# Kernel tuning notes

Measured on AMD Instinct MI355X. Metric: run time of the kernel, lower is better.

Reference implementation:

```python
import jax, jax.numpy as jnp
import numpy as np

N_NODES = 50000
N_EDGES = 600000
D = 128
H = 128


def setup_inputs() -> dict:
    key = jax.random.key(0)
    k1, k2, k3, k4 = jax.random.split(key, 4)
    x = jax.random.normal(k1, (N_NODES, D), dtype=jnp.float32)
    edge_index = jax.random.randint(k2, (2, N_EDGES), 0, N_NODES, dtype=jnp.int64)
    # Glorot-ish init for the two linear layers of SAGEConv
    scale = 1.0 / np.sqrt(D)
    W_l = jax.random.normal(k3, (H, D), dtype=jnp.float32) * scale
    b_l = jnp.zeros((H,), dtype=jnp.float32)
    W_r = jax.random.normal(k4, (H, D), dtype=jnp.float32) * scale
    return {"x": x, "edge_index": edge_index, "W_l": W_l, "b_l": b_l, "W_r": W_r}


def reference(x, edge_index, W_l, b_l, W_r):
    # PyG SAGEConv (aggr='mean', root_weight=True):
    #   out[i] = lin_l( mean_{j->i} x[j] ) + lin_r( x[i] )
    # edge_index[0] = source nodes (j), edge_index[1] = destination nodes (i)
    src = edge_index[0]
    dst = edge_index[1]
    n = x.shape[0]
    msgs = x[src]  # [E, D] gather
    agg_sum = jax.ops.segment_sum(msgs, dst, num_segments=n)  # [N, D]
    deg = jax.ops.segment_sum(jnp.ones((src.shape[0],), dtype=x.dtype), dst, num_segments=n)
    agg = agg_sum / jnp.maximum(deg, 1.0)[:, None]  # mean aggregation; 0 for isolated nodes
    out = agg @ W_l.T + b_l + x @ W_r.T  # [N, H]
    return out
```

## Files before the change

### kernel.cpp

```cpp
#include <hip/hip_runtime.h>
#include <hip/hip_bf16.h>

using f32x4 = __attribute__((ext_vector_type(4))) float;
using s16x8 = __attribute__((ext_vector_type(8))) short;

static __device__ __forceinline__ float bflo2f(unsigned int w) {
    union { unsigned int u; float f; } c; c.u = w << 16; return c.f;
}
static __device__ __forceinline__ float bfhi2f(unsigned int w) {
    union { unsigned int u; float f; } c; c.u = w & 0xffff0000u; return c.f;
}
static __device__ __forceinline__ unsigned int f2bf(float f) {
    union { float f; unsigned int u; } c; c.f = f;
    unsigned int u = c.u;
    u = u + 0x7fffu + ((u >> 16) & 1u);
    return u >> 16;
}

#define CAP 64

__global__ __launch_bounds__(256) void k_convert(
        const float* __restrict__ x, unsigned short* __restrict__ xb,
        const float* __restrict__ Wr, const float* __restrict__ Wl,
        s16x8* __restrict__ wprep, int* __restrict__ cnt, int* __restrict__ ovfn,
        int n4, int nxb, int N)
{
    int b = blockIdx.x;
    if (b < nxb) {
        int t = b * 256 + threadIdx.x;
        if (t >= n4) return;
        float4 v = ((const float4*)x)[t];
        ushort4 o;
        o.x = (unsigned short)f2bf(v.x);
        o.y = (unsigned short)f2bf(v.y);
        o.z = (unsigned short)f2bf(v.z);
        o.w = (unsigned short)f2bf(v.w);
        ((ushort4*)xb)[t] = o;
    } else if (b < nxb + 16) {
        int s = (b - nxb) * 256 + threadIdx.x;
        if (s >= 4096) return;
        int f = s >> 6, il = s & 63;
        int nt = f >> 3, ks = f & 7;
        int col = nt * 16 + (il & 15);
        int k   = ks * 32 + (il >> 4) * 8;
        const float* Wsrc = (k < 128) ? Wr : Wl;
        int k0 = k & 127;
        const float4* wp = (const float4*)(Wsrc + (size_t)col * 128 + k0);
        float4 w0 = wp[0], w1 = wp[1];
        s16x8 v;
        v[0] = (short)f2bf(w0.x); v[1] = (short)f2bf(w0.y);
        v[2] = (short)f2bf(w0.z); v[3] = (short)f2bf(w0.w);
        v[4] = (short)f2bf(w1.x); v[5] = (short)f2bf(w1.y);
        v[6] = (short)f2bf(w1.z); v[7] = (short)f2bf(w1.w);
        wprep[s] = v;
    } else {
        int z = (b - nxb - 16) * 256 + threadIdx.x;
        if (z == 0) *ovfn = 0;
        int base = z * 4;
        if (base + 4 <= N) {
            ((int4*)cnt)[z] = make_int4(0, 0, 0, 0);
        } else if (base < N) {
            for (int i = base; i < N; ++i) cnt[i] = 0;
        }
    }
}

__global__ __launch_bounds__(256) void k_bucket(
        const int* __restrict__ src, const int* __restrict__ dst,
        int* __restrict__ cnt, int* __restrict__ slot,
        int* __restrict__ ovfn, int* __restrict__ ovf, int E)
{
    int e = blockIdx.x * 256 + threadIdx.x;
    if (e >= E) return;
    int d = dst[e];
    int p = atomicAdd(&cnt[d], 1);
    if (p < CAP) {
        slot[(size_t)d * CAP + p] = src[e];
    } else {
        int q = atomicAdd(ovfn, 1);
        ovf[2 * q]     = d;
        ovf[2 * q + 1] = src[e];
    }
}

__global__ __launch_bounds__(256) void k_gather_wide(
        const uint4* __restrict__ xq, const int* __restrict__ slot,
        const int* __restrict__ cnt, const int* __restrict__ ovfn,
        const int* __restrict__ ovf, uint4* __restrict__ abq, int N)
{
    int d    = blockIdx.x * 4 + (threadIdx.x >> 6);
    int lane = threadIdx.x & 63;
    if (d >= N) return;
    int m  = cnt[d];
    int n1 = min(m, CAP);
    const int* sl = slot + (size_t)d * CAP;
    int c = lane & 15, r = lane >> 4;
    float a0=0,a1=0,a2=0,a3=0,a4=0,a5=0,a6=0,a7=0;
    const uint4 z4 = {0u, 0u, 0u, 0u};
    for (int p = 0; p < n1; p += 16) {
        int pe0 = p + r, pe1 = p + 4 + r, pe2 = p + 8 + r, pe3 = p + 12 + r;
        uint4 v0 = z4, v1 = z4, v2 = z4, v3 = z4;
        if (pe0 < n1) v0 = xq[(size_t)sl[pe0] * 16 + c];
        if (pe1 < n1) v1 = xq[(size_t)sl[pe1] * 16 + c];
        if (pe2 < n1) v2 = xq[(size_t)sl[pe2] * 16 + c];
        if (pe3 < n1) v3 = xq[(size_t)sl[pe3] * 16 + c];
        a0 += bflo2f(v0.x); a1 += bfhi2f(v0.x);
        a2 += bflo2f(v0.y); a3 += bfhi2f(v0.y);
        a4 += bflo2f(v0.z); a5 += bfhi2f(v0.z);
        a6 += bflo2f(v0.w); a7 += bfhi2f(v0.w);
        a0 += bflo2f(v1.x); a1 += bfhi2f(v1.x);
        a2 += bflo2f(v1.y); a3 += bfhi2f(v1.y);
        a4 += bflo2f(v1.z); a5 += bfhi2f(v1.z);
        a6 += bflo2f(v1.w); a7 += bfhi2f(v1.w);
        a0 += bflo2f(v2.x); a1 += bfhi2f(v2.x);
        a2 += bflo2f(v2.y); a3 += bfhi2f(v2.y);
        a4 += bflo2f(v2.z); a5 += bfhi2f(v2.z);
        a6 += bflo2f(v2.w); a7 += bfhi2f(v2.w);
        a0 += bflo2f(v3.x); a1 += bfhi2f(v3.x);
        a2 += bflo2f(v3.y); a3 += bfhi2f(v3.y);
        a4 += bflo2f(v3.z); a5 += bfhi2f(v3.z);
        a6 += bflo2f(v3.w); a7 += bfhi2f(v3.w);
    }
    if (m > CAP) {
        int nov = *ovfn;
        for (int k = 0; k < nov; ++k) {
            if (ovf[2 * k] == d && r == 0) {
                uint4 v = xq[(size_t)ovf[2 * k + 1] * 16 + c];
                a0 += bflo2f(v.x); a1 += bfhi2f(v.x);
                a2 += bflo2f(v.y); a3 += bfhi2f(v.y);
                a4 += bflo2f(v.z); a5 += bfhi2f(v.z);
                a6 += bflo2f(v.w); a7 += bfhi2f(v.w);
            }
        }
    }
    a0 += __shfl_xor(a0, 16, 64); a0 += __shfl_xor(a0, 32, 64);
    a1 += __shfl_xor(a1, 16, 64); a1 += __shfl_xor(a1, 32, 64);
    a2 += __shfl_xor(a2, 16, 64); a2 += __shfl_xor(a2, 32, 64);
    a3 += __shfl_xor(a3, 16, 64); a3 += __shfl_xor(a3, 32, 64);
    a4 += __shfl_xor(a4, 16, 64); a4 += __shfl_xor(a4, 32, 64);
    a5 += __shfl_xor(a5, 16, 64); a5 += __shfl_xor(a5, 32, 64);
    a6 += __shfl_xor(a6, 16, 64); a6 += __shfl_xor(a6, 32, 64);
    a7 += __shfl_xor(a7, 16, 64); a7 += __shfl_xor(a7, 32, 64);
    if (r == 0) {
        float inv = 1.0f / (float)max(m, 1);
        uint4 o;
        o.x = f2bf(a0 * inv) | (f2bf(a1 * inv) << 16);
        o.y = f2bf(a2 * inv) | (f2bf(a3 * inv) << 16);
        o.z = f2bf(a4 * inv) | (f2bf(a5 * inv) << 16);
        o.w = f2bf(a6 * inv) | (f2bf(a7 * inv) << 16);
        abq[(size_t)d * 16 + c] = o;
    }
}

__global__ __launch_bounds__(256) void k_combine_mfma(
        const unsigned short* __restrict__ xb, const unsigned short* __restrict__ ab,
        const s16x8* __restrict__ wprep,
        const float* __restrict__ bl,
        float* __restrict__ out, int N, int T)
{
    __shared__ s16x8 Bf[64][64];
    int t = threadIdx.x;
    {
        const uint4* ws = (const uint4*)wprep;
        uint4* bd = (uint4*)&Bf[0][0];
        for (int s = t; s < 4096; s += 256) bd[s] = ws[s];
    }
    __syncthreads();

    int wid = t >> 6, l = t & 63;
    int lr = l & 15, lg = l >> 4;
    float bias[8];
    #pragma unroll
    for (int nt = 0; nt < 8; ++nt) bias[nt] = bl[nt * 16 + lr];

    for (int tile = blockIdx.x; tile < T; tile += gridDim.x) {
        int rb0 = tile * 128 + wid * 32;
        int rb1 = rb0 + 16;
        int ar0 = min(rb0 + lr, N - 1);
        int ar1 = min(rb1 + lr, N - 1);
        const s16x8* xr0 = (const s16x8*)(xb + (size_t)ar0 * 128);
        const s16x8* ag0 = (const s16x8*)(ab + (size_t)ar0 * 128);
        const s16x8* xr1 = (const s16x8*)(xb + (size_t)ar1 * 128);
        const s16x8* ag1 = (const s16x8*)(ab + (size_t)ar1 * 128);
        s16x8 af0[8], af1[8];
        #pragma unroll
        for (int ks = 0; ks < 4; ++ks) {
            af0[ks]     = xr0[ks * 4 + lg];
            af0[4 + ks] = ag0[ks * 4 + lg];
            af1[ks]     = xr1[ks * 4 + lg];
            af1[4 + ks] = ag1[ks * 4 + lg];
        }

        f32x4 acc0[8], acc1[8];
        #pragma unroll
        for (int nt = 0; nt < 8; ++nt) {
            float b = bias[nt];
            acc0[nt] = (f32x4){b, b, b, b};
            acc1[nt] = (f32x4){b, b, b, b};
        }

        #pragma unroll
        for (int ks = 0; ks < 8; ++ks)
            #pragma unroll
            for (int nt = 0; nt < 8; ++nt) {
                s16x8 bfrag = Bf[nt * 8 + ks][l];
                acc0[nt] = __builtin_amdgcn_mfma_f32_16x16x32_bf16(
                               af0[ks], bfrag, acc0[nt], 0, 0, 0);
                acc1[nt] = __builtin_amdgcn_mfma_f32_16x16x32_bf16(
                               af1[ks], bfrag, acc1[nt], 0, 0, 0);
            }

        #pragma unroll
        for (int i = 0; i < 4; ++i) {
            int row0 = rb0 + lg * 4 + i;
            if (row0 < N) {
                float* op = out + (size_t)row0 * 128 + lr;
                #pragma unroll
                for (int nt = 0; nt < 8; ++nt) op[nt * 16] = acc0[nt][i];
            }
            int row1 = rb1 + lg * 4 + i;
            if (row1 < N) {
                float* op = out + (size_t)row1 * 128 + lr;
                #pragma unroll
                for (int nt = 0; nt < 8; ++nt) op[nt * 16] = acc1[nt][i];
            }
        }
    }
}


__global__ __launch_bounds__(256) void k_scatter_legacy(
        const float* __restrict__ x,
        const int* __restrict__ src, const int* __restrict__ dst,
        float* __restrict__ agg, float* __restrict__ deg, int E)
{
    int e    = (int)((blockIdx.x * 256u + threadIdx.x) >> 6);
    int lane = threadIdx.x & 63;
    if (e >= E) return;
    int s = src[e];
    int d = dst[e];
    float2 v = ((const float2*)(x + (size_t)s * 128u))[lane];
    float* ar = agg + (size_t)d * 128u;
    unsafeAtomicAdd(ar + 2 * lane,     v.x);
    unsafeAtomicAdd(ar + 2 * lane + 1, v.y);
    if (lane == 0) unsafeAtomicAdd(deg + d, 1.0f);
}

__global__ __launch_bounds__(256) void k_combine_legacy(
        const float* __restrict__ x, const float* agg, const float* __restrict__ deg,
        const float* __restrict__ Wr, const float* __restrict__ Wl,
        const float* __restrict__ bl,
        float* out, int N)
{
    __shared__ uint4 WT4[64][64];
    for (int idx = threadIdx.x; idx < 64 * 64; idx += 256) {
        int g = idx >> 6, l = idx & 63;
        uint4 wv;
        unsigned int* wp = &wv.x;
        #pragma unroll
        for (int kk = 0; kk < 4; ++kk) {
            int k = g * 4 + kk;
            const float* Wsrc = (k < 128) ? Wr : Wl;
            int km = k & 127;
            unsigned int lo = f2bf(Wsrc[(size_t)l * 128 + km]);
            unsigned int hi = f2bf(Wsrc[(size_t)(l + 64) * 128 + km]);
            wp[kk] = lo | (hi << 16);
        }
        WT4[g][l] = wv;
    }
    __syncthreads();

    int wid = threadIdx.x >> 6, lane = threadIdx.x & 63;
    float b0 = bl[lane], b1 = bl[lane + 64];
    for (int row = blockIdx.x * 4 + wid; row < N; row += gridDim.x * 4) {
        const float4* xr = (const float4*)(x   + (size_t)row * 128);
        const float4* ar = (const float4*)(agg + (size_t)row * 128);
        float inv = 1.0f / fmaxf(deg[row], 1.0f);
        float acc0 = b0, acc1 = b1;
        #pragma unroll 8
        for (int c = 0; c < 32; ++c) {
            uint4 w4 = WT4[c][lane];
            float4 q = xr[c];
            #pragma unroll
            for (int j = 0; j < 4; ++j) {
                unsigned int w = (&w4.x)[j];
                float f = (&q.x)[j];
                acc0 = fmaf(f, bflo2f(w), acc0);
                acc1 = fmaf(f, bfhi2f(w), acc1);
            }
        }
        #pragma unroll 8
        for (int c = 0; c < 32; ++c) {
            uint4 w4 = WT4[c + 32][lane];
            float4 q = ar[c];
            #pragma unroll
            for (int j = 0; j < 4; ++j) {
                unsigned int w = (&w4.x)[j];
                float f = (&q.x)[j] * inv;
                acc0 = fmaf(f, bflo2f(w), acc0);
                acc1 = fmaf(f, bfhi2f(w), acc1);
            }
        }
        out[(size_t)row * 128 + lane]      = acc0;
        out[(size_t)row * 128 + lane + 64] = acc1;
    }
}


extern "C" void kernel_launch(void* const* d_in, const int* in_sizes, int n_in,
                              void* d_out, int out_size, void* d_ws, size_t ws_size,
                              hipStream_t stream)
{
    const float* x  = (const float*)d_in[0];
    const int*   ei = (const int*)d_in[1];
    const float* Wl = (const float*)d_in[2];
    const float* bl = (const float*)d_in[3];
    const float* Wr = (const float*)d_in[4];
    float*      out = (float*)d_out;

    int N = in_sizes[0] / 128;
    int E = in_sizes[1] / 2;
    const int* src = ei;
    const int* dst = ei + E;

    size_t bfB = (size_t)N * 128 * 2;

    size_t nInts = (size_t)N + 64 + 2 * (size_t)E + (size_t)N * CAP;
    size_t intsB = ((nInts * 4) + 255) & ~(size_t)255;

    if (ws_size >= intsB + 2 * bfB + 65536) {
        int* cnt  = (int*)d_ws;
        int* ovfn = cnt + N;
        int* ovf  = ovfn + 64;
        int* slot = ovf + 2 * (size_t)E;
        unsigned short* xb = (unsigned short*)((char*)d_ws + intsB);
        unsigned short* ab = xb + (size_t)N * 128;
        s16x8* wprep = (s16x8*)((char*)ab + bfB);

        int nxb = (N * 32 + 255) / 256;
        int nzb = ((N + 3) / 4 + 255) / 256;
        int ncv = nxb + 16 + nzb;

        k_convert   <<<ncv, 256, 0, stream>>>(x, xb, Wr, Wl, wprep, cnt, ovfn,
                                              N * 32, nxb, N);
        k_bucket    <<<(E + 255) / 256, 256, 0, stream>>>(src, dst, cnt, slot,
                                                          ovfn, ovf, E);
        k_gather_wide<<<(N + 3) / 4, 256, 0, stream>>>(
                (const uint4*)xb, slot, cnt, ovfn, ovf, (uint4*)ab, N);
        int T = (N + 127) / 128;
        k_combine_mfma<<<T, 256, 0, stream>>>(xb, ab, wprep, bl, out, N, T);
    } else {
        float* agg = out;
        float* deg = (float*)d_ws;
        hipMemsetAsync(out, 0, (size_t)N * 128 * 4, stream);
        hipMemsetAsync(deg, 0, (size_t)N * 4, stream);
        k_scatter_legacy<<<(E + 3) / 4, 256, 0, stream>>>(x, src, dst, agg, deg, E);
        k_combine_legacy<<<1024, 256, 0, stream>>>(x, agg, deg, Wr, Wl, bl, out, N);
    }
}
```

Before: 93.57 us.

## Fuse edge bucketing with bf16 conversion; shrink bucket capacity to 32

Moves counter zeroing into a small kernel of its own and merges the edge-bucketing pass with the x/weight bf16 conversion into one launch, so the atomic-heavy scatter and the bandwidth-bound conversion can overlap on the GPU. It also halves the per-node slot capacity from 64 to 32, which shrinks the slot array and its footprint. The kernel count stays the same. The smaller capacity may route more edges to the overflow path, though with about 12 edges per node on average that should be rare.

```diff
diff --git a/kernel.cpp b/kernel.cpp
--- a/kernel.cpp
+++ b/kernel.cpp
@@ -17,17 +17,45 @@
     return u >> 16;
 }
 
-#define CAP 64
-
-__global__ __launch_bounds__(256) void k_convert(
+#define CAP 32
+
+__global__ __launch_bounds__(256) void k_zero(
+        int* __restrict__ cnt, int* __restrict__ ovfn, int N)
+{
+    int z = blockIdx.x * 256 + threadIdx.x;
+    if (z == 0) *ovfn = 0;
+    int base = z * 4;
+    if (base + 4 <= N) {
+        ((int4*)cnt)[z] = make_int4(0, 0, 0, 0);
+    } else if (base < N) {
+        for (int i = base; i < N; ++i) cnt[i] = 0;
+    }
+}
+
+__global__ __launch_bounds__(256) void k_fused(
+        const int* __restrict__ src, const int* __restrict__ dst,
+        int* __restrict__ cnt, int* __restrict__ slot,
+        int* __restrict__ ovfn, int* __restrict__ ovf,
         const float* __restrict__ x, unsigned short* __restrict__ xb,
         const float* __restrict__ Wr, const float* __restrict__ Wl,
-        s16x8* __restrict__ wprep, int* __restrict__ cnt, int* __restrict__ ovfn,
-        int n4, int nxb, int N)
+        s16x8* __restrict__ wprep,
+        int E, int n4, int nbk, int nxb)
 {
     int b = blockIdx.x;
-    if (b < nxb) {
-        int t = b * 256 + threadIdx.x;
+    if (b < nbk) {
+        int e = b * 256 + threadIdx.x;
+        if (e >= E) return;
+        int d = dst[e];
+        int p = atomicAdd(&cnt[d], 1);
+        if (p < CAP) {
+            slot[(size_t)d * CAP + p] = src[e];
+        } else {
+            int q = atomicAdd(ovfn, 1);
+            ovf[2 * q]     = d;
+            ovf[2 * q + 1] = src[e];
+        }
+    } else if (b < nbk + nxb) {
+        int t = (b - nbk) * 256 + threadIdx.x;
         if (t >= n4) return;
         float4 v = ((const float4*)x)[t];
         ushort4 o;
@@ -36,8 +64,8 @@
         o.z = (unsigned short)f2bf(v.z);
         o.w = (unsigned short)f2bf(v.w);
         ((ushort4*)xb)[t] = o;
-    } else if (b < nxb + 16) {
-        int s = (b - nxb) * 256 + threadIdx.x;
+    } else {
+        int s = (b - nbk - nxb) * 256 + threadIdx.x;
         if (s >= 4096) return;
         int f = s >> 6, il = s & 63;
         int nt = f >> 3, ks = f & 7;
@@ -53,33 +81,6 @@
         v[4] = (short)f2bf(w1.x); v[5] = (short)f2bf(w1.y);
         v[6] = (short)f2bf(w1.z); v[7] = (short)f2bf(w1.w);
         wprep[s] = v;
-    } else {
-        int z = (b - nxb - 16) * 256 + threadIdx.x;
-        if (z == 0) *ovfn = 0;
-        int base = z * 4;
-        if (base + 4 <= N) {
-            ((int4*)cnt)[z] = make_int4(0, 0, 0, 0);
-        } else if (base < N) {
-            for (int i = base; i < N; ++i) cnt[i] = 0;
-        }
-    }
-}
-
-__global__ __launch_bounds__(256) void k_bucket(
-        const int* __restrict__ src, const int* __restrict__ dst,
-        int* __restrict__ cnt, int* __restrict__ slot,
-        int* __restrict__ ovfn, int* __restrict__ ovf, int E)
-{
-    int e = blockIdx.x * 256 + threadIdx.x;
-    if (e >= E) return;
-    int d = dst[e];
-    int p = atomicAdd(&cnt[d], 1);
-    if (p < CAP) {
-        slot[(size_t)d * CAP + p] = src[e];
-    } else {
-        int q = atomicAdd(ovfn, 1);
-        ovf[2 * q]     = d;
-        ovf[2 * q + 1] = src[e];
     }
 }
 
@@ -337,14 +338,15 @@
         unsigned short* ab = xb + (size_t)N * 128;
         s16x8* wprep = (s16x8*)((char*)ab + bfB);
 
+        int nz  = ((N + 3) / 4 + 255) / 256;
+        int nbk = (E + 255) / 256;
         int nxb = (N * 32 + 255) / 256;
-        int nzb = ((N + 3) / 4 + 255) / 256;
-        int ncv = nxb + 16 + nzb;
-
-        k_convert   <<<ncv, 256, 0, stream>>>(x, xb, Wr, Wl, wprep, cnt, ovfn,
-                                              N * 32, nxb, N);
-        k_bucket    <<<(E + 255) / 256, 256, 0, stream>>>(src, dst, cnt, slot,
-                                                          ovfn, ovf, E);
+        int nfb = nbk + nxb + 16;
+
+        k_zero <<<nz, 256, 0, stream>>>(cnt, ovfn, N);
+        k_fused<<<nfb, 256, 0, stream>>>(src, dst, cnt, slot, ovfn, ovf,
+                                         x, xb, Wr, Wl, wprep,
+                                         E, N * 32, nbk, nxb);
         k_gather_wide<<<(N + 3) / 4, 256, 0, stream>>>(
                 (const uint4*)xb, slot, cnt, ovfn, ovf, (uint4*)ab, N);
         int T = (N + 127) / 128;
```

New measurement: 95.27 us. No clear change (+1.8%).

## Replace per-node atomic bucketing with two-pass block-binned counting sort into CSR

Applied to the files above, without the earlier changes.

Builds the destination-grouped edge list with a two-level counting sort: edges are first binned into 256-node coarse bins, using shared-memory histograms and one global atomic per bin per block, then each bin is sorted locally into a compact CSR with offsets and degrees. This replaces one global atomic per edge plus a sparse fixed-capacity slot array, and cuts the counter-zeroing work. In exchange it adds a kernel launch and a second pass over the edges. Every gather now scans the whole overflow list, which could be expensive if bins overflow.

```diff
diff --git a/kernel.cpp b/kernel.cpp
--- a/kernel.cpp
+++ b/kernel.cpp
@@ -17,13 +17,13 @@
     return u >> 16;
 }
 
-#define CAP 64
+#define ET 8
 
 __global__ __launch_bounds__(256) void k_convert(
         const float* __restrict__ x, unsigned short* __restrict__ xb,
         const float* __restrict__ Wr, const float* __restrict__ Wl,
-        s16x8* __restrict__ wprep, int* __restrict__ cnt, int* __restrict__ ovfn,
-        int n4, int nxb, int N)
+        s16x8* __restrict__ wprep, int* __restrict__ bcnt, int* __restrict__ ovfn,
+        int n4, int nxb)
 {
     int b = blockIdx.x;
     if (b < nxb) {
@@ -54,56 +54,119 @@
         v[6] = (short)f2bf(w1.z); v[7] = (short)f2bf(w1.w);
         wprep[s] = v;
     } else {
-        int z = (b - nxb - 16) * 256 + threadIdx.x;
-        if (z == 0) *ovfn = 0;
-        int base = z * 4;
-        if (base + 4 <= N) {
-            ((int4*)cnt)[z] = make_int4(0, 0, 0, 0);
-        } else if (base < N) {
-            for (int i = base; i < N; ++i) cnt[i] = 0;
-        }
-    }
-}
-
-__global__ __launch_bounds__(256) void k_bucket(
+        int t = threadIdx.x;
+        bcnt[t] = 0;
+        if (t == 0) *ovfn = 0;
+    }
+}
+
+__global__ __launch_bounds__(256) void k_bin(
         const int* __restrict__ src, const int* __restrict__ dst,
-        int* __restrict__ cnt, int* __restrict__ slot,
-        int* __restrict__ ovfn, int* __restrict__ ovf, int E)
-{
-    int e = blockIdx.x * 256 + threadIdx.x;
-    if (e >= E) return;
-    int d = dst[e];
-    int p = atomicAdd(&cnt[d], 1);
-    if (p < CAP) {
-        slot[(size_t)d * CAP + p] = src[e];
-    } else {
-        int q = atomicAdd(ovfn, 1);
-        ovf[2 * q]     = d;
-        ovf[2 * q + 1] = src[e];
+        int* __restrict__ bcnt, unsigned int* __restrict__ binbuf,
+        int* __restrict__ ovfn, int* __restrict__ ovf,
+        int E, int NB, int capb)
+{
+    __shared__ int hist[256];
+    __shared__ int base[256];
+    int t = threadIdx.x;
+    hist[t] = 0;
+    __syncthreads();
+    int e0 = blockIdx.x * (256 * ET);
+    int bins[ET], pls[ET];
+    unsigned int pay[ET];
+    #pragma unroll
+    for (int i = 0; i < ET; ++i) {
+        int e = e0 + t + i * 256;
+        bins[i] = -1;
+        if (e < E) {
+            int d = dst[e];
+            int s = src[e];
+            bins[i] = d >> 8;
+            pay[i]  = ((unsigned int)(d & 255) << 24) | (unsigned int)s;
+            pls[i]  = atomicAdd(&hist[bins[i]], 1);
+        }
+    }
+    __syncthreads();
+    if (t < NB && hist[t] > 0) base[t] = atomicAdd(&bcnt[t], hist[t]);
+    __syncthreads();
+    #pragma unroll
+    for (int i = 0; i < ET; ++i) {
+        if (bins[i] >= 0) {
+            int pos = base[bins[i]] + pls[i];
+            if (pos < capb) {
+                binbuf[(size_t)bins[i] * capb + pos] = pay[i];
+            } else {
+                int q = atomicAdd(ovfn, 1);
+                ovf[2 * q]     = (bins[i] << 8) | (int)(pay[i] >> 24);
+                ovf[2 * q + 1] = (int)(pay[i] & 0xFFFFFFu);
+            }
+        }
+    }
+}
+
+__global__ __launch_bounds__(256) void k_sort(
+        const int* __restrict__ bcnt, const unsigned int* __restrict__ binbuf,
+        int* __restrict__ srcS, int* __restrict__ offg, int* __restrict__ degg,
+        int N, int capb)
+{
+    __shared__ int cnt[256];
+    __shared__ int sh[256];
+    __shared__ int cur[256];
+    int b = blockIdx.x, t = threadIdx.x;
+    int m = min(bcnt[b], capb);
+    cnt[t] = 0;
+    __syncthreads();
+    const unsigned int* bb = binbuf + (size_t)b * capb;
+    for (int j = t; j < m; j += 256)
+        atomicAdd(&cnt[bb[j] >> 24], 1);
+    __syncthreads();
+    int v = cnt[t];
+    sh[t] = v;
+    __syncthreads();
+    #pragma unroll
+    for (int d2 = 1; d2 < 256; d2 <<= 1) {
+        int y = (t >= d2) ? sh[t - d2] : 0;
+        __syncthreads();
+        sh[t] += y;
+        __syncthreads();
+    }
+    int off = sh[t] - v;
+    cur[t] = off;
+    int node = b * 256 + t;
+    if (node < N) {
+        offg[node] = b * capb + off;
+        degg[node] = v;
+    }
+    __syncthreads();
+    for (int j = t; j < m; j += 256) {
+        unsigned int c = bb[j];
+        int p = atomicAdd(&cur[c >> 24], 1);
+        srcS[(size_t)b * capb + p] = (int)(c & 0xFFFFFFu);
     }
 }
 
 __global__ __launch_bounds__(256) void k_gather_wide(
-        const uint4* __restrict__ xq, const int* __restrict__ slot,
-        const int* __restrict__ cnt, const int* __restrict__ ovfn,
-        const int* __restrict__ ovf, uint4* __restrict__ abq, int N)
+        const uint4* __restrict__ xq, const int* __restrict__ srcS,
+        const int* __restrict__ offg, const int* __restrict__ degg,
+        const int* __restrict__ ovfn, const int* __restrict__ ovf,
+        uint4* __restrict__ abq, int N)
 {
     int d    = blockIdx.x * 4 + (threadIdx.x >> 6);
     int lane = threadIdx.x & 63;
     if (d >= N) return;
-    int m  = cnt[d];
-    int n1 = min(m, CAP);
-    const int* sl = slot + (size_t)d * CAP;
+    int n0 = offg[d];
+    int m0 = degg[d];
+    const int* sl = srcS + n0;
     int c = lane & 15, r = lane >> 4;
     float a0=0,a1=0,a2=0,a3=0,a4=0,a5=0,a6=0,a7=0;
     const uint4 z4 = {0u, 0u, 0u, 0u};
-    for (int p = 0; p < n1; p += 16) {
+    for (int p = 0; p < m0; p += 16) {
         int pe0 = p + r, pe1 = p + 4 + r, pe2 = p + 8 + r, pe3 = p + 12 + r;
         uint4 v0 = z4, v1 = z4, v2 = z4, v3 = z4;
-        if (pe0 < n1) v0 = xq[(size_t)sl[pe0] * 16 + c];
-        if (pe1 < n1) v1 = xq[(size_t)sl[pe1] * 16 + c];
-        if (pe2 < n1) v2 = xq[(size_t)sl[pe2] * 16 + c];
-        if (pe3 < n1) v3 = xq[(size_t)sl[pe3] * 16 + c];
+        if (pe0 < m0) v0 = xq[(size_t)sl[pe0] * 16 + c];
+        if (pe1 < m0) v1 = xq[(size_t)sl[pe1] * 16 + c];
+        if (pe2 < m0) v2 = xq[(size_t)sl[pe2] * 16 + c];
+        if (pe3 < m0) v3 = xq[(size_t)sl[pe3] * 16 + c];
         a0 += bflo2f(v0.x); a1 += bfhi2f(v0.x);
         a2 += bflo2f(v0.y); a3 += bfhi2f(v0.y);
         a4 += bflo2f(v0.z); a5 += bfhi2f(v0.z);
@@ -121,10 +184,12 @@
         a4 += bflo2f(v3.z); a5 += bfhi2f(v3.z);
         a6 += bflo2f(v3.w); a7 += bfhi2f(v3.w);
     }
-    if (m > CAP) {
-        int nov = *ovfn;
-        for (int k = 0; k < nov; ++k) {
-            if (ovf[2 * k] == d && r == 0) {
+    int deg = m0;
+    int nov = *ovfn;
+    for (int k = 0; k < nov; ++k) {
+        if (ovf[2 * k] == d) {
+            ++deg;
+            if (r == 0) {
                 uint4 v = xq[(size_t)ovf[2 * k + 1] * 16 + c];
                 a0 += bflo2f(v.x); a1 += bfhi2f(v.x);
                 a2 += bflo2f(v.y); a3 += bfhi2f(v.y);
@@ -142,7 +207,7 @@
     a6 += __shfl_xor(a6, 16, 64); a6 += __shfl_xor(a6, 32, 64);
     a7 += __shfl_xor(a7, 16, 64); a7 += __shfl_xor(a7, 32, 64);
     if (r == 0) {
-        float inv = 1.0f / (float)max(m, 1);
+        float inv = 1.0f / (float)max(deg, 1);
         uint4 o;
         o.x = f2bf(a0 * inv) | (f2bf(a1 * inv) << 16);
         o.y = f2bf(a2 * inv) | (f2bf(a3 * inv) << 16);
@@ -323,30 +388,38 @@
     const int* src = ei;
     const int* dst = ei + E;
 
+    int NB   = (N + 255) >> 8;
+    int capb = ((2 * E / (NB > 0 ? NB : 1)) + 255) & ~255;
     size_t bfB = (size_t)N * 128 * 2;
 
-    size_t nInts = (size_t)N + 64 + 2 * (size_t)E + (size_t)N * CAP;
+    size_t nInts = 256 + 64 + 2 * (size_t)E + 2 * (size_t)NB * capb
+                 + 2 * (size_t)N;
     size_t intsB = ((nInts * 4) + 255) & ~(size_t)255;
 
-    if (ws_size >= intsB + 2 * bfB + 65536) {
-        int* cnt  = (int*)d_ws;
-        int* ovfn = cnt + N;
+    if (ws_size >= intsB + 2 * bfB + 65536 && NB <= 256 && N < (1 << 24)) {
+        int* bcnt = (int*)d_ws;
+        int* ovfn = bcnt + 256;
         int* ovf  = ovfn + 64;
-        int* slot = ovf + 2 * (size_t)E;
+        unsigned int* binbuf = (unsigned int*)(ovf + 2 * (size_t)E);
+        int* srcS = (int*)(binbuf + (size_t)NB * capb);
+        int* offg = srcS + (size_t)NB * capb;
+        int* degg = offg + N;
         unsigned short* xb = (unsigned short*)((char*)d_ws + intsB);
         unsigned short* ab = xb + (size_t)N * 128;
         s16x8* wprep = (s16x8*)((char*)ab + bfB);
 
         int nxb = (N * 32 + 255) / 256;
-        int nzb = ((N + 3) / 4 + 255) / 256;
-        int ncv = nxb + 16 + nzb;
-
-        k_convert   <<<ncv, 256, 0, stream>>>(x, xb, Wr, Wl, wprep, cnt, ovfn,
-                                              N * 32, nxb, N);
-        k_bucket    <<<(E + 255) / 256, 256, 0, stream>>>(src, dst, cnt, slot,
-                                                          ovfn, ovf, E);
+        int ncv = nxb + 16 + 1;
+        int nbin = (E + 256 * ET - 1) / (256 * ET);
+
+        k_convert<<<ncv, 256, 0, stream>>>(x, xb, Wr, Wl, wprep, bcnt, ovfn,
+                                           N * 32, nxb);
+        k_bin    <<<nbin, 256, 0, stream>>>(src, dst, bcnt, binbuf, ovfn, ovf,
+                                            E, NB, capb);
+        k_sort   <<<NB, 256, 0, stream>>>(bcnt, binbuf, srcS, offg, degg,
+                                          N, capb);
         k_gather_wide<<<(N + 3) / 4, 256, 0, stream>>>(
-                (const uint4*)xb, slot, cnt, ovfn, ovf, (uint4*)ab, N);
+                (const uint4*)xb, srcS, offg, degg, ovfn, ovf, (uint4*)ab, N);
         int T = (N + 127) / 128;
         k_combine_mfma<<<T, 256, 0, stream>>>(xb, ab, wprep, bl, out, N, T);
     } else {
```

After: 83.66 us, median of 2. 1.12x faster.
